# Performance work log

Hardware: AMD Instinct MI355X
Metric: run time of the kernel (lower is better)

Reference implementation:

```python
import jax, jax.numpy as jnp
import numpy as np
import math

TEXT_EMBEDDING_DIM = 768.0
SEQ = 81
DIM = 64
B, H = 256, 16


def setup_inputs() -> dict:
    key = jax.random.key(0)
    kq, kk, kv, ke = jax.random.split(key, 4)
    Q = jax.random.normal(kq, (B, H, SEQ, DIM), dtype=jnp.float32)
    K = jax.random.normal(kk, (B, H, SEQ, DIM), dtype=jnp.float32)
    V = jax.random.normal(kv, (B, H, SEQ, DIM), dtype=jnp.float32)
    emb_table = jax.random.normal(ke, (2 * SEQ + 1, DIM), dtype=jnp.float32)
    return {"Q": Q, "K": K, "V": V, "emb_table": emb_table, "use_causal": 1}


def reference(Q, K, V, emb_table, use_causal):
    S = Q.shape[-2]
    # relative index matrix: rel[i, j] = (S - 1 + i) - j, in [0, 2S-2]
    rel = jnp.arange(S - 1, 2 * S - 1)[:, None] - jnp.arange(S)  # [S, S] int
    emb = emb_table[rel]  # [S, S, d]
    # QK^T plus learned relative-position bias
    eij = jnp.einsum('bhid,bhjd->bhij', Q, K) + jnp.einsum('bhid,ijd->bhij', Q, emb)
    attn = eij / math.sqrt(TEXT_EMBEDDING_DIM)  # note: sqrt(768), not sqrt(dim), per source
    if use_causal:
        i = jnp.arange(S)[:, None]
        j = jnp.arange(S)
        mask = jnp.where(i >= j, 0.0, -1000000000.0).astype(attn.dtype)  # [S, S]
        attn = attn + mask
    attn = jax.nn.softmax(attn, axis=-1)
    return jnp.einsum('bhij,bhjd->bhid', attn, V)
```

## Files before the change

### kernel.cpp

```cpp
#include <hip/hip_runtime.h>

#define SEQ 81
#define SP 96
#define DIM 64
#define NT 384
#define NW 6

typedef short bf16x8  __attribute__((ext_vector_type(8)));
typedef short short4v __attribute__((ext_vector_type(4)));
typedef float f32x4   __attribute__((ext_vector_type(4)));

static constexpr float kScale = 0.03608439182435161f;

__device__ __forceinline__ short f2bf(float f) {
    unsigned u = __builtin_bit_cast(unsigned, f);
    u = (u + 0x7FFFu + ((u >> 16) & 1u)) >> 16;
    return (short)u;
}
__device__ __forceinline__ float bf2f(short h) {
    unsigned u = ((unsigned)(unsigned short)h) << 16;
    return __builtin_bit_cast(float, u);
}

__global__ void emb_cvt_kernel(const float* __restrict__ in, short* __restrict__ out, int n) {
    int i = blockIdx.x * 256 + threadIdx.x;
    if (i < n) out[i] = f2bf(in[i]);
}

__global__ __launch_bounds__(NT, 6)
void rpsa_kernel(const float* __restrict__ Q, const float* __restrict__ K,
                 const float* __restrict__ V, const short* __restrict__ embw,
                 const int* __restrict__ ucp, float* __restrict__ out)
{
    extern __shared__ char smraw[];
    short* sQ  = (short*)smraw;
    short* sK  = sQ + SP*DIM;
    short* sVt = sK + SP*DIM;
    short* sP  = sQ;

    const int tid = threadIdx.x;
    const size_t base = (size_t)blockIdx.x * (SEQ * DIM);
    const int uc = ucp[0];

    for (int u = tid; u < SP * DIM / 8; u += NT) {
        const int row = u >> 3;
        const int so  = (u & 7) * 8;
        bf16x8 qb = {0,0,0,0,0,0,0,0}, kb = {0,0,0,0,0,0,0,0};
        if (row < SEQ) {
            const f32x4 q0 = *(const f32x4*)(Q + base + row*DIM + so);
            const f32x4 q1 = *(const f32x4*)(Q + base + row*DIM + so + 4);
            const f32x4 k0 = *(const f32x4*)(K + base + row*DIM + so);
            const f32x4 k1 = *(const f32x4*)(K + base + row*DIM + so + 4);
            #pragma unroll
            for (int t = 0; t < 4; ++t) {
                qb[t] = f2bf(q0[t]); qb[4+t] = f2bf(q1[t]);
                kb[t] = f2bf(k0[t]); kb[4+t] = f2bf(k1[t]);
            }
        }
        const int idx = row*DIM + (so ^ (8*(row&7)));
        *(bf16x8*)(sQ + idx) = qb;
        *(bf16x8*)(sK + idx) = kb;
    }
    {
        const int j4 = tid >> 4;
        const int d4 = tid & 15;
        f32x4 rw[4];
        #pragma unroll
        for (int e = 0; e < 4; ++e) {
            const int j = 4*j4 + e;
            rw[e] = (j < SEQ) ? *(const f32x4*)(V + base + j*DIM + 4*d4)
                              : (f32x4){0.f,0.f,0.f,0.f};
        }
        #pragma unroll
        for (int c = 0; c < 4; ++c) {
            const int d = 4*d4 + c;
            short4v pv = { f2bf(rw[0][c]), f2bf(rw[1][c]), f2bf(rw[2][c]), f2bf(rw[3][c]) };
            *(short4v*)(sVt + d*128 + ((4*j4) ^ (8*(d&7)))) = pv;
        }
    }
    __syncthreads();

    const int w  = tid >> 6, L = tid & 63;
    const int lr = L & 15,  lg = L >> 4;
    const int i0 = 16*w + 4*lg;

    bf16x8 aq0, aq1;
    {
        const int row = 16*w + lr;
        aq0 = *(const bf16x8*)(sQ + row*DIM + ((8*lg)      ^ (8*(row&7))));
        aq1 = *(const bf16x8*)(sQ + row*DIM + ((32 + 8*lg) ^ (8*(row&7))));
    }

    f32x4 accs[NW] = {};
    const int ntEnd = uc ? w : (NW - 1);
    #pragma unroll
    for (int nt = 0; nt < NW; ++nt) {
        if (nt > ntEnd) continue;
        const int row = 16*nt + lr;
        bf16x8 b0 = *(const bf16x8*)(sK + row*DIM + ((8*lg)      ^ (8*(row&7))));
        bf16x8 b1 = *(const bf16x8*)(sK + row*DIM + ((32 + 8*lg) ^ (8*(row&7))));
        f32x4 a = accs[nt];
        a = __builtin_amdgcn_mfma_f32_16x16x32_bf16(aq0, b0, a, 0, 0, 0);
        a = __builtin_amdgcn_mfma_f32_16x16x32_bf16(aq1, b1, a, 0, 0, 0);
        accs[nt] = a;
    }
    __syncthreads();

    #pragma unroll
    for (int nt = 0; nt < NW; ++nt) {
        if (nt > w) continue;
        int erow = (SEQ - 1) + 16*nt + lr;
        if (erow > 2*SEQ) erow = 2*SEQ;
        bf16x8 b0 = *(const bf16x8*)(embw + erow*DIM + 8*lg);
        bf16x8 b1 = *(const bf16x8*)(embw + erow*DIM + 32 + 8*lg);
        f32x4 a = {0.f,0.f,0.f,0.f};
        a = __builtin_amdgcn_mfma_f32_16x16x32_bf16(aq0, b0, a, 0, 0, 0);
        a = __builtin_amdgcn_mfma_f32_16x16x32_bf16(aq1, b1, a, 0, 0, 0);
        #pragma unroll
        for (int r = 0; r < 4; ++r) {
            const int i = i0 + r;
            const int j = i - (16*nt + lr);
            if (j >= 0) sP[i*128 + (j ^ (8*(i&7)))] = f2bf(a[r] * kScale);
        }
    }
    if (!uc) {
        #pragma unroll
        for (int nt = 0; nt < NW; ++nt) {
            if (nt < w) continue;
            const int erow = 16*nt + lr;
            bf16x8 b0 = *(const bf16x8*)(embw + erow*DIM + 8*lg);
            bf16x8 b1 = *(const bf16x8*)(embw + erow*DIM + 32 + 8*lg);
            f32x4 a = {0.f,0.f,0.f,0.f};
            a = __builtin_amdgcn_mfma_f32_16x16x32_bf16(aq0, b0, a, 0, 0, 0);
            a = __builtin_amdgcn_mfma_f32_16x16x32_bf16(aq1, b1, a, 0, 0, 0);
            #pragma unroll
            for (int r = 0; r < 4; ++r) {
                const int i  = i0 + r;
                const int rp = 16*nt + lr;
                if (rp >= i && rp < SEQ - 1)
                    sP[i*128 + ((SEQ - 1 + i - rp) ^ (8*(i&7)))] = f2bf(a[r] * kScale);
            }
        }
    }

    float x[NW][4];
    float mr[4] = {-1e30f, -1e30f, -1e30f, -1e30f};
    #pragma unroll
    for (int nt = 0; nt < NW; ++nt) {
        const bool live = (!uc) || (nt <= w);
        const int j = 16*nt + lr;
        #pragma unroll
        for (int r = 0; r < 4; ++r) {
            const int i = i0 + r;
            float v = accs[nt][r] * kScale;
            if (live) v += bf2f(sP[i*128 + (j ^ (8*(i&7)))]);
            x[nt][r] = v;
            const int jl = uc ? (i < SEQ-1 ? i : SEQ-1) : (SEQ-1);
            if (j <= jl) mr[r] = fmaxf(mr[r], v);
        }
    }
    #pragma unroll
    for (int r = 0; r < 4; ++r) {
        float m = mr[r];
        m = fmaxf(m, __shfl_xor(m, 1, 16));
        m = fmaxf(m, __shfl_xor(m, 2, 16));
        m = fmaxf(m, __shfl_xor(m, 4, 16));
        m = fmaxf(m, __shfl_xor(m, 8, 16));
        mr[r] = m;
    }
    float sr[4] = {0.f, 0.f, 0.f, 0.f};
    #pragma unroll
    for (int nt = 0; nt < NW; ++nt) {
        const int j = 16*nt + lr;
        #pragma unroll
        for (int r = 0; r < 4; ++r) {
            const int i = i0 + r;
            const int jl = uc ? (i < SEQ-1 ? i : SEQ-1) : (SEQ-1);
            const float e = (j <= jl) ? __expf(x[nt][r] - mr[r]) : 0.f;
            x[nt][r] = e; sr[r] += e;
        }
    }
    #pragma unroll
    for (int r = 0; r < 4; ++r) {
        float s = sr[r];
        s += __shfl_xor(s, 1, 16);
        s += __shfl_xor(s, 2, 16);
        s += __shfl_xor(s, 4, 16);
        s += __shfl_xor(s, 8, 16);
        sr[r] = 1.f / s;
    }
    #pragma unroll
    for (int nt = 0; nt < NW; ++nt) {
        const int j = 16*nt + lr;
        #pragma unroll
        for (int r = 0; r < 4; ++r) {
            const int i = i0 + r;
            sP[i*128 + (j ^ (8*(i&7)))] = f2bf(x[nt][r] * sr[r]);
        }
    }

    bf16x8 ap0, ap1, ap2;
    {
        const int row = 16*w + lr;
        ap0 = *(const bf16x8*)(sP + row*128 + ((8*lg)      ^ (8*(row&7))));
        ap1 = *(const bf16x8*)(sP + row*128 + ((32 + 8*lg) ^ (8*(row&7))));
        ap2 = *(const bf16x8*)(sP + row*128 + ((64 + 8*lg) ^ (8*(row&7))));
    }
    #pragma unroll
    for (int nt = 0; nt < 4; ++nt) {
        const int d = 16*nt + lr;
        bf16x8 b0 = *(const bf16x8*)(sVt + d*128 + ((8*lg)      ^ (8*(d&7))));
        bf16x8 b1 = *(const bf16x8*)(sVt + d*128 + ((32 + 8*lg) ^ (8*(d&7))));
        bf16x8 b2 = *(const bf16x8*)(sVt + d*128 + ((64 + 8*lg) ^ (8*(d&7))));
        f32x4 a = {0.f,0.f,0.f,0.f};
        a = __builtin_amdgcn_mfma_f32_16x16x32_bf16(ap0, b0, a, 0, 0, 0);
        a = __builtin_amdgcn_mfma_f32_16x16x32_bf16(ap1, b1, a, 0, 0, 0);
        a = __builtin_amdgcn_mfma_f32_16x16x32_bf16(ap2, b2, a, 0, 0, 0);
        #pragma unroll
        for (int r = 0; r < 4; ++r) {
            const int i = i0 + r;
            if (i < SEQ) out[base + i*DIM + 16*nt + lr] = a[r];
        }
    }
}

extern "C" void kernel_launch(void* const* d_in, const int* in_sizes, int n_in,
                              void* d_out, int out_size, void* d_ws, size_t ws_size,
                              hipStream_t stream) {
    const float* Q   = (const float*)d_in[0];
    const float* K   = (const float*)d_in[1];
    const float* V   = (const float*)d_in[2];
    const float* emb = (const float*)d_in[3];
    const int*   uc  = (const int*)d_in[4];
    float* out = (float*)d_out;

    const int nbh   = in_sizes[0] / (SEQ * DIM);
    const int n_emb = in_sizes[3];

    short* embw = (short*)d_ws;
    emb_cvt_kernel<<<(n_emb + 255) / 256, 256, 0, stream>>>(emb, embw, n_emb);

    const size_t smem = (size_t)(SP*DIM*2 + DIM*128) * sizeof(short);
    hipFuncSetAttribute(reinterpret_cast<const void*>(rpsa_kernel),
                        hipFuncAttributeMaxDynamicSharedMemorySize, (int)smem);
    rpsa_kernel<<<nbh, NT, smem, stream>>>(Q, K, V, embw, uc, out);
}
```

Measured before the change: 92.94 us.

## Load Q directly into registers, pad LDS rows, shrink shared memory for occupancy

Q is now read from global memory straight into MFMA A-operand registers, with the softmax scale folded in before the bf16 conversion, so the Q staging buffer in LDS is gone. K, V^T and P use padded row strides instead of XOR swizzles, and the P buffer aliases the K region. Shared memory drops from about 40KB to 32KB and launch bounds rise to 8 blocks per CU, aiming for higher occupancy. In exchange, each 16-byte fragment load is split into two 8-byte LDS reads, and rounding differs slightly because the scale is applied before Q is converted to bf16.

After: 86.82 us. 1.07x faster.

```diff
diff --git a/kernel.cpp b/kernel.cpp
--- a/kernel.cpp
+++ b/kernel.cpp
@@ -1,14 +1,17 @@
 #include <hip/hip_runtime.h>
 
 #define SEQ 81
-#define SP 96
+#define SP  96
 #define DIM 64
-#define NT 384
-#define NW 6
-
-typedef short bf16x8  __attribute__((ext_vector_type(8)));
-typedef short short4v __attribute__((ext_vector_type(4)));
-typedef float f32x4   __attribute__((ext_vector_type(4)));
+#define NT  384
+#define NW  6
+#define LDK 68
+#define LDV 100
+#define LDP 100
+
+typedef short bf16x8 __attribute__((ext_vector_type(8)));
+typedef short bf16x4 __attribute__((ext_vector_type(4)));
+typedef float f32x4  __attribute__((ext_vector_type(4)));
 
 static constexpr float kScale = 0.03608439182435161f;
 
@@ -21,45 +24,63 @@
     unsigned u = ((unsigned)(unsigned short)h) << 16;
     return __builtin_bit_cast(float, u);
 }
+__device__ __forceinline__ bf16x8 cat8(bf16x4 a, bf16x4 b) {
+    bf16x8 r;
+    r[0]=a[0]; r[1]=a[1]; r[2]=a[2]; r[3]=a[3];
+    r[4]=b[0]; r[5]=b[1]; r[6]=b[2]; r[7]=b[3];
+    return r;
+}
 
 __global__ void emb_cvt_kernel(const float* __restrict__ in, short* __restrict__ out, int n) {
     int i = blockIdx.x * 256 + threadIdx.x;
     if (i < n) out[i] = f2bf(in[i]);
 }
 
-__global__ __launch_bounds__(NT, 6)
+__global__ __launch_bounds__(NT, 8)
 void rpsa_kernel(const float* __restrict__ Q, const float* __restrict__ K,
                  const float* __restrict__ V, const short* __restrict__ embw,
                  const int* __restrict__ ucp, float* __restrict__ out)
 {
     extern __shared__ char smraw[];
-    short* sQ  = (short*)smraw;
-    short* sK  = sQ + SP*DIM;
-    short* sVt = sK + SP*DIM;
-    short* sP  = sQ;
+    short* sVt = (short*)smraw;
+    short* sK  = (short*)(smraw + 12800);
+    short* sP  = (short*)(smraw + 12800);
 
     const int tid = threadIdx.x;
     const size_t base = (size_t)blockIdx.x * (SEQ * DIM);
     const int uc = ucp[0];
+    const int w  = tid >> 6, L = tid & 63;
+    const int lr = L & 15,  lg = L >> 4;
+    const int i0 = 16*w + 4*lg;
+
+    bf16x8 aq0, aq1;
+    {
+        const int qrow = (16*w + lr < SEQ) ? (16*w + lr) : (SEQ - 1);
+        const float* qp = Q + base + qrow*DIM + 8*lg;
+        const f32x4 q0 = *(const f32x4*)(qp);
+        const f32x4 q1 = *(const f32x4*)(qp + 4);
+        const f32x4 q2 = *(const f32x4*)(qp + 32);
+        const f32x4 q3 = *(const f32x4*)(qp + 36);
+        #pragma unroll
+        for (int t = 0; t < 4; ++t) {
+            aq0[t]   = f2bf(q0[t]*kScale);
+            aq0[4+t] = f2bf(q1[t]*kScale);
+            aq1[t]   = f2bf(q2[t]*kScale);
+            aq1[4+t] = f2bf(q3[t]*kScale);
+        }
+    }
 
     for (int u = tid; u < SP * DIM / 8; u += NT) {
-        const int row = u >> 3;
-        const int so  = (u & 7) * 8;
-        bf16x8 qb = {0,0,0,0,0,0,0,0}, kb = {0,0,0,0,0,0,0,0};
+        const int row = u >> 3, so = (u & 7) * 8;
+        bf16x4 lo = {0,0,0,0}, hi = {0,0,0,0};
         if (row < SEQ) {
-            const f32x4 q0 = *(const f32x4*)(Q + base + row*DIM + so);
-            const f32x4 q1 = *(const f32x4*)(Q + base + row*DIM + so + 4);
             const f32x4 k0 = *(const f32x4*)(K + base + row*DIM + so);
             const f32x4 k1 = *(const f32x4*)(K + base + row*DIM + so + 4);
             #pragma unroll
-            for (int t = 0; t < 4; ++t) {
-                qb[t] = f2bf(q0[t]); qb[4+t] = f2bf(q1[t]);
-                kb[t] = f2bf(k0[t]); kb[4+t] = f2bf(k1[t]);
-            }
-        }
-        const int idx = row*DIM + (so ^ (8*(row&7)));
-        *(bf16x8*)(sQ + idx) = qb;
-        *(bf16x8*)(sK + idx) = kb;
+            for (int t = 0; t < 4; ++t) { lo[t] = f2bf(k0[t]); hi[t] = f2bf(k1[t]); }
+        }
+        *(bf16x4*)(sK + row*LDK + so)     = lo;
+        *(bf16x4*)(sK + row*LDK + so + 4) = hi;
     }
     {
         const int j4 = tid >> 4;
@@ -74,31 +95,22 @@
         #pragma unroll
         for (int c = 0; c < 4; ++c) {
             const int d = 4*d4 + c;
-            short4v pv = { f2bf(rw[0][c]), f2bf(rw[1][c]), f2bf(rw[2][c]), f2bf(rw[3][c]) };
-            *(short4v*)(sVt + d*128 + ((4*j4) ^ (8*(d&7)))) = pv;
+            bf16x4 pv = { f2bf(rw[0][c]), f2bf(rw[1][c]), f2bf(rw[2][c]), f2bf(rw[3][c]) };
+            *(bf16x4*)(sVt + d*LDV + 4*j4) = pv;
         }
     }
     __syncthreads();
-
-    const int w  = tid >> 6, L = tid & 63;
-    const int lr = L & 15,  lg = L >> 4;
-    const int i0 = 16*w + 4*lg;
-
-    bf16x8 aq0, aq1;
-    {
-        const int row = 16*w + lr;
-        aq0 = *(const bf16x8*)(sQ + row*DIM + ((8*lg)      ^ (8*(row&7))));
-        aq1 = *(const bf16x8*)(sQ + row*DIM + ((32 + 8*lg) ^ (8*(row&7))));
-    }
 
     f32x4 accs[NW] = {};
     const int ntEnd = uc ? w : (NW - 1);
     #pragma unroll
     for (int nt = 0; nt < NW; ++nt) {
         if (nt > ntEnd) continue;
-        const int row = 16*nt + lr;
-        bf16x8 b0 = *(const bf16x8*)(sK + row*DIM + ((8*lg)      ^ (8*(row&7))));
-        bf16x8 b1 = *(const bf16x8*)(sK + row*DIM + ((32 + 8*lg) ^ (8*(row&7))));
+        const int kr = 16*nt + lr;
+        bf16x8 b0 = cat8(*(const bf16x4*)(sK + kr*LDK + 8*lg),
+                         *(const bf16x4*)(sK + kr*LDK + 8*lg + 4));
+        bf16x8 b1 = cat8(*(const bf16x4*)(sK + kr*LDK + 32 + 8*lg),
+                         *(const bf16x4*)(sK + kr*LDK + 32 + 8*lg + 4));
         f32x4 a = accs[nt];
         a = __builtin_amdgcn_mfma_f32_16x16x32_bf16(aq0, b0, a, 0, 0, 0);
         a = __builtin_amdgcn_mfma_f32_16x16x32_bf16(aq1, b1, a, 0, 0, 0);
@@ -120,7 +132,7 @@
         for (int r = 0; r < 4; ++r) {
             const int i = i0 + r;
             const int j = i - (16*nt + lr);
-            if (j >= 0) sP[i*128 + (j ^ (8*(i&7)))] = f2bf(a[r] * kScale);
+            if (j >= 0) sP[i*LDP + j] = f2bf(a[r]);
         }
     }
     if (!uc) {
@@ -138,12 +150,11 @@
                 const int i  = i0 + r;
                 const int rp = 16*nt + lr;
                 if (rp >= i && rp < SEQ - 1)
-                    sP[i*128 + ((SEQ - 1 + i - rp) ^ (8*(i&7)))] = f2bf(a[r] * kScale);
+                    sP[i*LDP + (SEQ - 1 + i - rp)] = f2bf(a[r]);
             }
         }
     }
 
-    float x[NW][4];
     float mr[4] = {-1e30f, -1e30f, -1e30f, -1e30f};
     #pragma unroll
     for (int nt = 0; nt < NW; ++nt) {
@@ -152,10 +163,10 @@
         #pragma unroll
         for (int r = 0; r < 4; ++r) {
             const int i = i0 + r;
-            float v = accs[nt][r] * kScale;
-            if (live) v += bf2f(sP[i*128 + (j ^ (8*(i&7)))]);
-            x[nt][r] = v;
-            const int jl = uc ? (i < SEQ-1 ? i : SEQ-1) : (SEQ-1);
+            float v = accs[nt][r];
+            if (live) v += bf2f(sP[i*LDP + j]);
+            accs[nt][r] = v;
+            const int jl = uc ? ((i < SEQ-1) ? i : SEQ-1) : (SEQ-1);
             if (j <= jl) mr[r] = fmaxf(mr[r], v);
         }
     }
@@ -175,9 +186,9 @@
         #pragma unroll
         for (int r = 0; r < 4; ++r) {
             const int i = i0 + r;
-            const int jl = uc ? (i < SEQ-1 ? i : SEQ-1) : (SEQ-1);
-            const float e = (j <= jl) ? __expf(x[nt][r] - mr[r]) : 0.f;
-            x[nt][r] = e; sr[r] += e;
+            const int jl = uc ? ((i < SEQ-1) ? i : SEQ-1) : (SEQ-1);
+            const float e = (j <= jl) ? __expf(accs[nt][r] - mr[r]) : 0.f;
+            accs[nt][r] = e; sr[r] += e;
         }
     }
     #pragma unroll
@@ -195,23 +206,29 @@
         #pragma unroll
         for (int r = 0; r < 4; ++r) {
             const int i = i0 + r;
-            sP[i*128 + (j ^ (8*(i&7)))] = f2bf(x[nt][r] * sr[r]);
+            sP[i*LDP + j] = f2bf(accs[nt][r] * sr[r]);
         }
     }
 
     bf16x8 ap0, ap1, ap2;
     {
         const int row = 16*w + lr;
-        ap0 = *(const bf16x8*)(sP + row*128 + ((8*lg)      ^ (8*(row&7))));
-        ap1 = *(const bf16x8*)(sP + row*128 + ((32 + 8*lg) ^ (8*(row&7))));
-        ap2 = *(const bf16x8*)(sP + row*128 + ((64 + 8*lg) ^ (8*(row&7))));
+        ap0 = cat8(*(const bf16x4*)(sP + row*LDP + 8*lg),
+                   *(const bf16x4*)(sP + row*LDP + 8*lg + 4));
+        ap1 = cat8(*(const bf16x4*)(sP + row*LDP + 32 + 8*lg),
+                   *(const bf16x4*)(sP + row*LDP + 32 + 8*lg + 4));
+        ap2 = cat8(*(const bf16x4*)(sP + row*LDP + 64 + 8*lg),
+                   *(const bf16x4*)(sP + row*LDP + 64 + 8*lg + 4));
     }
     #pragma unroll
     for (int nt = 0; nt < 4; ++nt) {
         const int d = 16*nt + lr;
-        bf16x8 b0 = *(const bf16x8*)(sVt + d*128 + ((8*lg)      ^ (8*(d&7))));
-        bf16x8 b1 = *(const bf16x8*)(sVt + d*128 + ((32 + 8*lg) ^ (8*(d&7))));
-        bf16x8 b2 = *(const bf16x8*)(sVt + d*128 + ((64 + 8*lg) ^ (8*(d&7))));
+        bf16x8 b0 = cat8(*(const bf16x4*)(sVt + d*LDV + 8*lg),
+                         *(const bf16x4*)(sVt + d*LDV + 8*lg + 4));
+        bf16x8 b1 = cat8(*(const bf16x4*)(sVt + d*LDV + 32 + 8*lg),
+                         *(const bf16x4*)(sVt + d*LDV + 32 + 8*lg + 4));
+        bf16x8 b2 = cat8(*(const bf16x4*)(sVt + d*LDV + 64 + 8*lg),
+                         *(const bf16x4*)(sVt + d*LDV + 64 + 8*lg + 4));
         f32x4 a = {0.f,0.f,0.f,0.f};
         a = __builtin_amdgcn_mfma_f32_16x16x32_bf16(ap0, b0, a, 0, 0, 0);
         a = __builtin_amdgcn_mfma_f32_16x16x32_bf16(ap1, b1, a, 0, 0, 0);
@@ -240,7 +257,7 @@
     short* embw = (short*)d_ws;
     emb_cvt_kernel<<<(n_emb + 255) / 256, 256, 0, stream>>>(emb, embw, n_emb);
 
-    const size_t smem = (size_t)(SP*DIM*2 + DIM*128) * sizeof(short);
+    const size_t smem = 32000;
     hipFuncSetAttribute(reinterpret_cast<const void*>(rpsa_kernel),
                         hipFuncAttributeMaxDynamicSharedMemorySize, (int)smem);
     rpsa_kernel<<<nbh, NT, smem, stream>>>(Q, K, V, embw, uc, out);
```
